# Optimization experiments

Measured on AMD Instinct MI355X. Metric: run time of the kernel, lower is better.

## Reference

```python
import jax, jax.numpy as jnp
import numpy as np

B, C, H, W = 4, 256, 64, 64
D = C // 8  # query/key projection dim


def setup_inputs() -> dict:
    key = jax.random.key(0)
    ks = jax.random.split(key, 8)
    s = 0.02
    return {
        "x": jax.random.normal(ks[0], (B, C, H, W), dtype=jnp.float32),
        "Wq": jax.random.normal(ks[1], (D, C), dtype=jnp.float32) * s,
        "bq": jax.random.normal(ks[2], (D,), dtype=jnp.float32) * s,
        "Wk": jax.random.normal(ks[3], (D, C), dtype=jnp.float32) * s,
        "bk": jax.random.normal(ks[4], (D,), dtype=jnp.float32) * s,
        "Wv": jax.random.normal(ks[5], (C, C), dtype=jnp.float32) * s,
        "bv": jax.random.normal(ks[6], (C,), dtype=jnp.float32) * s,
        "gamma": jax.random.normal(ks[7], (1,), dtype=jnp.float32),
    }


def reference(x, Wq, bq, Wk, bk, Wv, bv, gamma):
    b, c, h, w = x.shape
    n = h * w
    xf = x.reshape(b, c, n)                                  # B,C,N
    # 1x1 convs == per-pixel linear projections
    q = jnp.einsum("dc,bcn->bdn", Wq, xf) + bq[None, :, None]  # B,D,N
    k = jnp.einsum("dc,bcn->bdn", Wk, xf) + bk[None, :, None]  # B,D,N
    v = jnp.einsum("ec,bcn->ben", Wv, xf) + bv[None, :, None]  # B,C,N
    # energy[b,i,j] = <q[:, i], k[:, j]>  (query index i, key index j)
    energy = jnp.einsum("bdi,bdj->bij", q, k)                # B,N,N
    attention = jax.nn.softmax(energy, axis=-1)              # softmax over keys j
    # out[b,c,i] = sum_j v[b,c,j] * attention[b,i,j]
    out = jnp.einsum("bcj,bij->bci", v, attention)           # B,C,N
    out = out.reshape(b, c, h, w)
    return gamma[0] * out + x
```

## Files before the change

kernel.cpp:

```cpp
#include <hip/hip_runtime.h>
#include <hip/hip_bf16.h>
#include <cstdint>

#define B_ 4
#define C_ 256
#define N_ 4096
#define D_ 32
#define LOG2E 1.44269504088896f

typedef __attribute__((ext_vector_type(8))) short bf16x8;
typedef __attribute__((ext_vector_type(4))) short s16x4;
typedef __attribute__((ext_vector_type(4))) float f32x4;

__device__ inline unsigned short f2bf(float f) {
    union { float f; uint32_t u; } v; v.f = f;
    uint32_t u = v.u;
    u += 0x7FFFu + ((u >> 16) & 1u);
    return (unsigned short)(u >> 16);
}

__device__ inline float exp2_raw(float x) {
    float r;
    asm("v_exp_f32 %0, %1" : "=v"(r) : "v"(x));
    return r;
}

__global__ __launch_bounds__(256) void wconv_kernel(
    const float* __restrict__ Wq, const float* __restrict__ Wk,
    const float* __restrict__ Wv, unsigned short* __restrict__ Wb)
{
    int i = (blockIdx.x * 256 + threadIdx.x) * 4;
    int r = i >> 8, k = i & 255;
    const float* src = (r < 32) ? Wq + r * 256 + k
                     : (r < 64) ? Wk + (r - 32) * 256 + k
                                : Wv + (r - 64) * 256 + k;
    f32x4 v = *reinterpret_cast<const f32x4*>(src);
    s16x4 o;
    #pragma unroll
    for (int j = 0; j < 4; ++j) o[j] = (short)f2bf(v[j]);
    *reinterpret_cast<s16x4*>(Wb + i) = o;
}

__global__ __launch_bounds__(256) void proj_kernel(
    const float* __restrict__ x, const unsigned short* __restrict__ Wb,
    const float* __restrict__ bq, const float* __restrict__ bk,
    const float* __restrict__ bv,
    unsigned short* __restrict__ Qt, unsigned short* __restrict__ Kt,
    unsigned short* __restrict__ V)
{
    __shared__ __align__(16) char smem[16384];
    const int t  = threadIdx.x;
    const int w  = t >> 6;
    const int l  = t & 63;
    const int lg = l >> 4;
    const int ll = l & 15;
    const int n0 = blockIdx.x * 32;
    const int b  = blockIdx.y;

    #pragma unroll
    for (int rep = 0; rep < 8; ++rep) {
        int flat = rep * 256 + t;
        int c = flat >> 3, chunk = flat & 7;
        f32x4 xv = *reinterpret_cast<const f32x4*>(
            x + ((size_t)(b * C_ + c)) * N_ + n0 + chunk * 4);
        #pragma unroll
        for (int j = 0; j < 4; ++j) {
            int n = chunk * 4 + j;
            *reinterpret_cast<unsigned short*>(
                smem + n * 512 + ((c * 2) ^ ((n & 7) << 4))) = f2bf(xv[j]);
        }
    }

    bf16x8 Af[5], Afn[5];
    #pragma unroll
    for (int rt = 0; rt < 5; ++rt) {
        int r = w * 80 + rt * 16 + ll;
        Af[rt] = *reinterpret_cast<const bf16x8*>(Wb + r * 256 + lg * 8);
    }

    f32x4 acc[5][2];
    #pragma unroll
    for (int rt = 0; rt < 5; ++rt)
        #pragma unroll
        for (int nt = 0; nt < 2; ++nt) acc[rt][nt] = (f32x4){0.f, 0.f, 0.f, 0.f};

    __syncthreads();

    for (int kc = 0; kc < 8; ++kc) {
        if (kc < 7) {
            #pragma unroll
            for (int rt = 0; rt < 5; ++rt) {
                int r = w * 80 + rt * 16 + ll;
                Afn[rt] = *reinterpret_cast<const bf16x8*>(
                    Wb + r * 256 + (kc + 1) * 32 + lg * 8);
            }
        }
        bf16x8 Bf[2];
        #pragma unroll
        for (int nt = 0; nt < 2; ++nt) {
            int n = nt * 16 + ll;
            Bf[nt] = *reinterpret_cast<const bf16x8*>(
                smem + n * 512 + ((kc * 64 + lg * 16) ^ ((n & 7) << 4)));
        }
        #pragma unroll
        for (int rt = 0; rt < 5; ++rt)
            #pragma unroll
            for (int nt = 0; nt < 2; ++nt)
                acc[rt][nt] = __builtin_amdgcn_mfma_f32_16x16x32_bf16(
                    Af[rt], Bf[nt], acc[rt][nt], 0, 0, 0);
        if (kc < 7) {
            #pragma unroll
            for (int rt = 0; rt < 5; ++rt) Af[rt] = Afn[rt];
        }
    }

    #pragma unroll
    for (int rt = 0; rt < 5; ++rt) {
        const int rrow = w * 80 + rt * 16 + lg * 4;
        float bias[4];
        #pragma unroll
        for (int q = 0; q < 4; ++q) {
            int rg = rrow + q;
            bias[q] = (rg < 32) ? bq[rg] : (rg < 64) ? bk[rg - 32] : bv[rg - 64];
        }
        if (rrow < 64) {
            const int d0 = rrow & 31;
            const bool isQ = (rrow < 32);
            unsigned short* dst = isQ ? Qt : Kt;
            #pragma unroll
            for (int nt = 0; nt < 2; ++nt) {
                int n = n0 + nt * 16 + ll;
                s16x4 sv;
                #pragma unroll
                for (int q = 0; q < 4; ++q) {
                    float v = acc[rt][nt][q] + bias[q];
                    if (isQ) v *= LOG2E;
                    sv[q] = (short)f2bf(v);
                }
                *reinterpret_cast<s16x4*>(dst + ((size_t)b * N_ + n) * D_ + d0) = sv;
            }
        } else {
            #pragma unroll
            for (int nt = 0; nt < 2; ++nt) {
                int n = n0 + nt * 16 + ll;
                #pragma unroll
                for (int q = 0; q < 4; ++q) {
                    int c = rrow - 64 + q;
                    V[((size_t)(b * C_ + c)) * N_ + n] = f2bf(acc[rt][nt][q] + bias[q]);
                }
            }
        }
    }
}

__device__ inline void stageV(const unsigned short* __restrict__ Vg, int b,
                              int j0, char* VsBuf, int w, int l) {
    #pragma unroll
    for (int i = 0; i < 4; ++i) {
        const int Lbyte = i * 8192 + w * 1024 + l * 16;
        const int c   = Lbyte >> 7;
        const int off = Lbyte & 127;
        const int src_off = off ^ ((c & 7) << 4);
        const unsigned short* src =
            Vg + ((size_t)(b * C_ + c)) * N_ + j0 + (src_off >> 1);
        char* dst = VsBuf + i * 8192 + w * 1024;
        __builtin_amdgcn_global_load_lds(
            (const __attribute__((address_space(1))) uint32_t*)src,
            (__attribute__((address_space(3))) uint32_t*)dst, 16, 0, 0);
    }
}

__global__ __launch_bounds__(512) void attn_kernel(
    const unsigned short* __restrict__ Qt, const unsigned short* __restrict__ Kt,
    const unsigned short* __restrict__ Vg, const float* __restrict__ x,
    const float* __restrict__ gamma, float* __restrict__ out)
{
    __shared__ __align__(16) char smem[74240];
    char* Pbase = smem + 65536;
    float* LbufF = reinterpret_cast<float*>(smem + 73728);
    const int t  = threadIdx.x;
    const int w  = t >> 6;
    const int l  = t & 63;
    const int lg = l >> 4;
    const int ll = l & 15;
    const int qt_p = w >> 2;
    const int jc   = w & 3;
    const int n0 = blockIdx.x * 32;
    const int b  = blockIdx.y;

    const bf16x8 qfrag = *reinterpret_cast<const bf16x8*>(
        Qt + ((size_t)b * N_ + n0 + qt_p * 16 + ll) * D_ + 8 * lg);

    f32x4 acc[2][2];
    #pragma unroll
    for (int qt = 0; qt < 2; ++qt)
        #pragma unroll
        for (int ct = 0; ct < 2; ++ct) acc[qt][ct] = (f32x4){0.f, 0.f, 0.f, 0.f};
    float l_lane[4] = {0.f, 0.f, 0.f, 0.f};

    stageV(Vg, b, 0, smem, w, l);
    bf16x8 kcur = *reinterpret_cast<const bf16x8*>(
        Kt + ((size_t)b * N_ + jc * 16 + ll) * D_ + 8 * lg);

    const f32x4 zero4 = {0.f, 0.f, 0.f, 0.f};

    for (int kt = 0; kt < 64; ++kt) {
        const int buf = kt & 1;
        const int ktn = (kt < 63) ? kt + 1 : 63;

        bf16x8 knxt = *reinterpret_cast<const bf16x8*>(
            Kt + ((size_t)b * N_ + ktn * 64 + jc * 16 + ll) * D_ + 8 * lg);

        f32x4 sf = __builtin_amdgcn_mfma_f32_16x16x32_bf16(qfrag, kcur, zero4, 0, 0, 0);

        float pv[4];
        #pragma unroll
        for (int r = 0; r < 4; ++r) {
            float p = exp2_raw(fminf(sf[r], 86.f));
            pv[r] = p;
            l_lane[r] += p;
        }

        char* Pw = Pbase + buf * 4096;
        #pragma unroll
        for (int r = 0; r < 4; ++r) {
            int row = qt_p * 16 + lg * 4 + r;
            int col = jc * 16 + ll;
            *reinterpret_cast<unsigned short*>(
                Pw + row * 128 + ((col * 2) ^ ((row & 7) << 4))) = f2bf(pv[r]);
        }

        asm volatile("s_waitcnt lgkmcnt(0)" ::: "memory");
        asm volatile("s_waitcnt vmcnt(1)" ::: "memory");
        __builtin_amdgcn_s_barrier();
        asm volatile("" ::: "memory");

        if (kt < 63)
            stageV(Vg, b, ktn * 64, smem + (buf ^ 1) * 32768, w, l);

        char* Pr = Pbase + buf * 4096;
        bf16x8 pfrag[2][2];
        #pragma unroll
        for (int qt = 0; qt < 2; ++qt)
            #pragma unroll
            for (int kh = 0; kh < 2; ++kh) {
                int row = qt * 16 + ll;
                pfrag[qt][kh] = *reinterpret_cast<const bf16x8*>(
                    Pr + row * 128 + ((kh * 64 + lg * 16) ^ ((row & 7) << 4)));
            }
        char* Vs = smem + buf * 32768;
        __builtin_amdgcn_s_setprio(1);
        #pragma unroll
        for (int ct = 0; ct < 2; ++ct) {
            int cl = w * 32 + ct * 16 + ll;
            #pragma unroll
            for (int kh = 0; kh < 2; ++kh) {
                bf16x8 vf = *reinterpret_cast<const bf16x8*>(
                    Vs + cl * 128 + ((kh * 64 + lg * 16) ^ ((cl & 7) << 4)));
                #pragma unroll
                for (int qt = 0; qt < 2; ++qt)
                    acc[qt][ct] = __builtin_amdgcn_mfma_f32_16x16x32_bf16(
                        pfrag[qt][kh], vf, acc[qt][ct], 0, 0, 0);
            }
        }
        __builtin_amdgcn_s_setprio(0);

        kcur = knxt;
    }

    #pragma unroll
    for (int off = 1; off < 16; off <<= 1)
        #pragma unroll
        for (int r = 0; r < 4; ++r)
            l_lane[r] += __shfl_xor(l_lane[r], off);
    if (ll == 0) {
        #pragma unroll
        for (int r = 0; r < 4; ++r) LbufF[w * 16 + lg * 4 + r] = l_lane[r];
    }
    __syncthreads();

    float inv[2][4];
    #pragma unroll
    for (int qt = 0; qt < 2; ++qt)
        #pragma unroll
        for (int r = 0; r < 4; ++r) {
            int lq = lg * 4 + r;
            float ls = LbufF[(qt * 4 + 0) * 16 + lq] + LbufF[(qt * 4 + 1) * 16 + lq]
                     + LbufF[(qt * 4 + 2) * 16 + lq] + LbufF[(qt * 4 + 3) * 16 + lq];
            inv[qt][r] = 1.f / ls;
        }

    #pragma unroll
    for (int qt = 0; qt < 2; ++qt)
        #pragma unroll
        for (int ct = 0; ct < 2; ++ct) {
            int cl = w * 32 + ct * 16 + ll;
            int ncol = qt * 16 + lg * 4;
            f32x4 v;
            #pragma unroll
            for (int r = 0; r < 4; ++r) v[r] = acc[qt][ct][r] * inv[qt][r];
            *reinterpret_cast<f32x4*>(smem + cl * 128 + ((ncol * 4) ^ ((cl & 7) << 4))) = v;
        }
    __syncthreads();

    const float g0 = gamma[0];
    #pragma unroll
    for (int p = 0; p < 4; ++p) {
        int li = p * 512 + t;
        int cl = li >> 3;
        int n4 = (li & 7) * 4;
        f32x4 ov = *reinterpret_cast<const f32x4*>(
            smem + cl * 128 + ((n4 * 4) ^ ((cl & 7) << 4)));
        size_t gi = ((size_t)(b * C_ + cl)) * N_ + n0 + n4;
        f32x4 xv = *reinterpret_cast<const f32x4*>(x + gi);
        f32x4 res;
        #pragma unroll
        for (int j = 0; j < 4; ++j) res[j] = g0 * ov[j] + xv[j];
        *reinterpret_cast<f32x4*>(out + gi) = res;
    }
}

extern "C" void kernel_launch(void* const* d_in, const int* in_sizes, int n_in,
                              void* d_out, int out_size, void* d_ws, size_t ws_size,
                              hipStream_t stream) {
    const float* x     = (const float*)d_in[0];
    const float* Wq    = (const float*)d_in[1];
    const float* bq    = (const float*)d_in[2];
    const float* Wk    = (const float*)d_in[3];
    const float* bk    = (const float*)d_in[4];
    const float* Wv    = (const float*)d_in[5];
    const float* bv    = (const float*)d_in[6];
    const float* gamma = (const float*)d_in[7];
    float* out = (float*)d_out;

    char* ws = (char*)d_ws;
    unsigned short* Qt = (unsigned short*)(ws);
    unsigned short* Kt = (unsigned short*)(ws + (1u << 20));
    unsigned short* V  = (unsigned short*)(ws + (2u << 20));
    unsigned short* Wb = (unsigned short*)(ws + (10u << 20));

    wconv_kernel<<<dim3(80), 256, 0, stream>>>(Wq, Wk, Wv, Wb);
    proj_kernel<<<dim3(N_ / 32, B_), 256, 0, stream>>>(
        x, Wb, bq, bk, bv, Qt, Kt, V);
    attn_kernel<<<dim3(N_ / 32, B_), 512, 0, stream>>>(
        Qt, Kt, V, x, gamma, out);
}
```

Measured before the change: 160.2 us.

## Stage V through registers into single LDS buffer and swizzle block ids

Replaces the double-buffered async global-to-LDS V staging with register prefetch one tile ahead and a single V buffer in LDS, adding a second barrier per iteration before overwriting it. This cuts LDS use roughly in half, which may allow more blocks per CU. Blocks are launched on a 1-D grid and remapped so consecutive block ids spread across XCDs while a batch's blocks share K/V in L2. It also removes the conditional on the weight prefetch in the projection kernel. The extra barrier and register-held V tile add sync cost and register pressure.

```diff
diff --git a/kernel.cpp b/kernel.cpp
--- a/kernel.cpp
+++ b/kernel.cpp
@@ -11,6 +11,7 @@
 typedef __attribute__((ext_vector_type(8))) short bf16x8;
 typedef __attribute__((ext_vector_type(4))) short s16x4;
 typedef __attribute__((ext_vector_type(4))) float f32x4;
+typedef __attribute__((ext_vector_type(4))) int i32x4;
 
 __device__ inline unsigned short f2bf(float f) {
     union { float f; uint32_t u; } v; v.f = f;
@@ -87,13 +88,12 @@
     __syncthreads();
 
     for (int kc = 0; kc < 8; ++kc) {
-        if (kc < 7) {
-            #pragma unroll
-            for (int rt = 0; rt < 5; ++rt) {
-                int r = w * 80 + rt * 16 + ll;
-                Afn[rt] = *reinterpret_cast<const bf16x8*>(
-                    Wb + r * 256 + (kc + 1) * 32 + lg * 8);
-            }
+        const int kcn = (kc + 1) & 7;
+        #pragma unroll
+        for (int rt = 0; rt < 5; ++rt) {
+            int r = w * 80 + rt * 16 + ll;
+            Afn[rt] = *reinterpret_cast<const bf16x8*>(
+                Wb + r * 256 + kcn * 32 + lg * 8);
         }
         bf16x8 Bf[2];
         #pragma unroll
@@ -108,10 +108,8 @@
             for (int nt = 0; nt < 2; ++nt)
                 acc[rt][nt] = __builtin_amdgcn_mfma_f32_16x16x32_bf16(
                     Af[rt], Bf[nt], acc[rt][nt], 0, 0, 0);
-        if (kc < 7) {
-            #pragma unroll
-            for (int rt = 0; rt < 5; ++rt) Af[rt] = Afn[rt];
-        }
+        #pragma unroll
+        for (int rt = 0; rt < 5; ++rt) Af[rt] = Afn[rt];
     }
 
     #pragma unroll
@@ -153,31 +151,14 @@
     }
 }
 
-__device__ inline void stageV(const unsigned short* __restrict__ Vg, int b,
-                              int j0, char* VsBuf, int w, int l) {
-    #pragma unroll
-    for (int i = 0; i < 4; ++i) {
-        const int Lbyte = i * 8192 + w * 1024 + l * 16;
-        const int c   = Lbyte >> 7;
-        const int off = Lbyte & 127;
-        const int src_off = off ^ ((c & 7) << 4);
-        const unsigned short* src =
-            Vg + ((size_t)(b * C_ + c)) * N_ + j0 + (src_off >> 1);
-        char* dst = VsBuf + i * 8192 + w * 1024;
-        __builtin_amdgcn_global_load_lds(
-            (const __attribute__((address_space(1))) uint32_t*)src,
-            (__attribute__((address_space(3))) uint32_t*)dst, 16, 0, 0);
-    }
-}
-
 __global__ __launch_bounds__(512) void attn_kernel(
     const unsigned short* __restrict__ Qt, const unsigned short* __restrict__ Kt,
     const unsigned short* __restrict__ Vg, const float* __restrict__ x,
     const float* __restrict__ gamma, float* __restrict__ out)
 {
-    __shared__ __align__(16) char smem[74240];
-    char* Pbase = smem + 65536;
-    float* LbufF = reinterpret_cast<float*>(smem + 73728);
+    __shared__ __align__(16) char smem[41472];
+    char* Pbase = smem + 32768;
+    float* LbufF = reinterpret_cast<float*>(smem + 40960);
     const int t  = threadIdx.x;
     const int w  = t >> 6;
     const int l  = t & 63;
@@ -185,8 +166,21 @@
     const int ll = l & 15;
     const int qt_p = w >> 2;
     const int jc   = w & 3;
-    const int n0 = blockIdx.x * 32;
-    const int b  = blockIdx.y;
+    const int bid  = blockIdx.x;
+    const int id   = (bid & 7) * 64 + (bid >> 3);
+    const int b    = id >> 7;
+    const int n0   = (id & 127) * 32;
+
+    const unsigned short* vsrc[4];
+    int vdst[4];
+    #pragma unroll
+    for (int i = 0; i < 4; ++i) {
+        int Lb  = i * 8192 + w * 1024 + l * 16;
+        int c   = Lb >> 7;
+        int off = Lb & 127;
+        vsrc[i] = Vg + ((size_t)(b * C_ + c)) * N_ + (off >> 1);
+        vdst[i] = c * 128 + (off ^ ((c & 7) << 4));
+    }
 
     const bf16x8 qfrag = *reinterpret_cast<const bf16x8*>(
         Qt + ((size_t)b * N_ + n0 + qt_p * 16 + ll) * D_ + 8 * lg);
@@ -198,14 +192,25 @@
         for (int ct = 0; ct < 2; ++ct) acc[qt][ct] = (f32x4){0.f, 0.f, 0.f, 0.f};
     float l_lane[4] = {0.f, 0.f, 0.f, 0.f};
 
-    stageV(Vg, b, 0, smem, w, l);
+    i32x4 vr[4];
+    #pragma unroll
+    for (int i = 0; i < 4; ++i) vr[i] = *reinterpret_cast<const i32x4*>(vsrc[i]);
+    #pragma unroll
+    for (int i = 0; i < 4; ++i) *reinterpret_cast<i32x4*>(smem + vdst[i]) = vr[i];
+    #pragma unroll
+    for (int i = 0; i < 4; ++i) vr[i] = *reinterpret_cast<const i32x4*>(vsrc[i] + 64);
+
     bf16x8 kcur = *reinterpret_cast<const bf16x8*>(
         Kt + ((size_t)b * N_ + jc * 16 + ll) * D_ + 8 * lg);
 
+    asm volatile("s_waitcnt lgkmcnt(0)" ::: "memory");
+    __builtin_amdgcn_s_barrier();
+    asm volatile("" ::: "memory");
+
     const f32x4 zero4 = {0.f, 0.f, 0.f, 0.f};
 
     for (int kt = 0; kt < 64; ++kt) {
-        const int buf = kt & 1;
+        const int pb  = kt & 1;
         const int ktn = (kt < 63) ? kt + 1 : 63;
 
         bf16x8 knxt = *reinterpret_cast<const bf16x8*>(
@@ -221,7 +226,7 @@
             l_lane[r] += p;
         }
 
-        char* Pw = Pbase + buf * 4096;
+        char* Pw = Pbase + pb * 4096;
         #pragma unroll
         for (int r = 0; r < 4; ++r) {
             int row = qt_p * 16 + lg * 4 + r;
@@ -231,14 +236,10 @@
         }
 
         asm volatile("s_waitcnt lgkmcnt(0)" ::: "memory");
-        asm volatile("s_waitcnt vmcnt(1)" ::: "memory");
         __builtin_amdgcn_s_barrier();
         asm volatile("" ::: "memory");
 
-        if (kt < 63)
-            stageV(Vg, b, ktn * 64, smem + (buf ^ 1) * 32768, w, l);
-
-        char* Pr = Pbase + buf * 4096;
+        char* Pr = Pbase + pb * 4096;
         bf16x8 pfrag[2][2];
         #pragma unroll
         for (int qt = 0; qt < 2; ++qt)
@@ -248,7 +249,6 @@
                 pfrag[qt][kh] = *reinterpret_cast<const bf16x8*>(
                     Pr + row * 128 + ((kh * 64 + lg * 16) ^ ((row & 7) << 4)));
             }
-        char* Vs = smem + buf * 32768;
         __builtin_amdgcn_s_setprio(1);
         #pragma unroll
         for (int ct = 0; ct < 2; ++ct) {
@@ -256,7 +256,7 @@
             #pragma unroll
             for (int kh = 0; kh < 2; ++kh) {
                 bf16x8 vf = *reinterpret_cast<const bf16x8*>(
-                    Vs + cl * 128 + ((kh * 64 + lg * 16) ^ ((cl & 7) << 4)));
+                    smem + cl * 128 + ((kh * 64 + lg * 16) ^ ((cl & 7) << 4)));
                 #pragma unroll
                 for (int qt = 0; qt < 2; ++qt)
                     acc[qt][ct] = __builtin_amdgcn_mfma_f32_16x16x32_bf16(
@@ -264,6 +264,21 @@
             }
         }
         __builtin_amdgcn_s_setprio(0);
+
+        asm volatile("s_waitcnt lgkmcnt(0)" ::: "memory");
+        __builtin_amdgcn_s_barrier();
+        asm volatile("" ::: "memory");
+
+        if (kt < 63) {
+            #pragma unroll
+            for (int i = 0; i < 4; ++i)
+                *reinterpret_cast<i32x4*>(smem + vdst[i]) = vr[i];
+            if (kt < 62) {
+                #pragma unroll
+                for (int i = 0; i < 4; ++i)
+                    vr[i] = *reinterpret_cast<const i32x4*>(vsrc[i] + (kt + 2) * 64);
+            }
+        }
 
         kcur = knxt;
     }
@@ -342,6 +357,6 @@
     wconv_kernel<<<dim3(80), 256, 0, stream>>>(Wq, Wk, Wv, Wb);
     proj_kernel<<<dim3(N_ / 32, B_), 256, 0, stream>>>(
         x, Wb, bq, bk, bv, Qt, Kt, V);
-    attn_kernel<<<dim3(N_ / 32, B_), 512, 0, stream>>>(
+    attn_kernel<<<dim3(512), 512, 0, stream>>>(
         Qt, Kt, V, x, gamma, out);
 }
```

Result: slower. 170.6 us (+6.5%).
